# Kernel optimization log

Measured on AMD Instinct MI355X. Metric: run time of the kernel, lower is better.

The kernel has to match this reference:

```python
import jax, jax.numpy as jnp
import numpy as np

N_NODES, N_EDGES, N_GRAPHS = 50000, 800000, 512
F_IN, HID, DIM_OUT = 128, 256, 16


def setup_inputs() -> dict:
    key = jax.random.key(0)
    ks = jax.random.split(key, 16)
    glorot = lambda k, fi, fo: jax.random.normal(k, (fi, fo), jnp.float32) * jnp.sqrt(2.0 / (fi + fo))
    return {
        "x": jax.random.normal(ks[0], (N_NODES, F_IN), jnp.float32),
        "edge_index": jax.random.randint(ks[1], (2, N_EDGES), 0, N_NODES, dtype=jnp.int32),
        "batch": jnp.sort(jax.random.randint(ks[2], (N_NODES,), 0, N_GRAPHS, dtype=jnp.int32)),
        "mol_wt": jax.random.uniform(ks[3], (N_GRAPHS, 1), jnp.float32),
        "n_rings": jax.random.uniform(ks[4], (N_GRAPHS, 1), jnp.float32),
        "W1": glorot(ks[5], F_IN, HID), "b1": jnp.zeros((HID,), jnp.float32),
        "W2": glorot(ks[6], HID, HID), "b2": jnp.zeros((HID,), jnp.float32),
        "W3": glorot(ks[7], HID, HID), "b3": jnp.zeros((HID,), jnp.float32),
        "fcW1": glorot(ks[8], HID + 2, 196), "fcb1": jnp.zeros((196,), jnp.float32),
        "fcW2": glorot(ks[9], 196, DIM_OUT), "fcb2": jnp.zeros((DIM_OUT,), jnp.float32),
    }


def _gcn_conv(x, W, b, src, dst, deg_inv_sqrt, n_nodes):
    # PyG GCNConv: linear transform, then D^-1/2 (A+I) D^-1/2 aggregation, then bias
    xw = x @ W  # [N, HID]
    norm = deg_inv_sqrt[src] * deg_inv_sqrt[dst]  # [E+N]
    msg = norm[:, None] * xw[src]  # gather + scale
    out = jax.ops.segment_sum(msg, dst, num_segments=n_nodes)  # scatter-add at targets
    return out + b


def reference(x, edge_index, batch, mol_wt, n_rings,
              W1, b1, W2, b2, W3, b3, fcW1, fcb1, fcW2, fcb2):
    n_nodes = x.shape[0]
    self_loop = jnp.arange(n_nodes, dtype=edge_index.dtype)
    src = jnp.concatenate([edge_index[0], self_loop])
    dst = jnp.concatenate([edge_index[1], self_loop])
    deg = jax.ops.segment_sum(jnp.ones_like(dst, dtype=x.dtype), dst, num_segments=n_nodes)
    deg_inv_sqrt = jnp.where(deg > 0, jax.lax.rsqrt(deg), 0.0)

    h = jax.nn.relu(_gcn_conv(x, W1, b1, src, dst, deg_inv_sqrt, n_nodes))
    h = jax.nn.relu(_gcn_conv(h, W2, b2, src, dst, deg_inv_sqrt, n_nodes))
    h = jax.nn.relu(_gcn_conv(h, W3, b3, src, dst, deg_inv_sqrt, n_nodes))

    n_graphs = mol_wt.shape[0]
    sums = jax.ops.segment_sum(h, batch, num_segments=n_graphs)
    counts = jax.ops.segment_sum(jnp.ones((n_nodes,), h.dtype), batch, num_segments=n_graphs)
    hg = sums / jnp.maximum(counts, 1.0)[:, None]  # global mean pool

    hg = jnp.concatenate([hg, mol_wt, n_rings], axis=1)  # [G, 258]
    hg = jax.nn.relu(hg @ fcW1 + fcb1)
    return hg @ fcW2 + fcb2
```

## Files before the change

### kernel.cpp

```cpp
#include <hip/hip_runtime.h>

#define NN 50000
#define NE 800000
#define NG 512
#define FIN 128
#define HID 256
#define NBUK 196

typedef short short8 __attribute__((ext_vector_type(8)));
typedef float f32x4 __attribute__((ext_vector_type(4)));

static inline int cdiv(int a, int b) { return (a + b - 1) / b; }

static __device__ inline unsigned short f2bf(float f) {
    unsigned int u = __float_as_uint(f);
    unsigned int r = (u + 0x7FFF + ((u >> 16) & 1)) >> 16;
    return (unsigned short)r;
}
static __device__ inline float bf2f(unsigned short h) {
    return __uint_as_float(((unsigned int)h) << 16);
}
static __device__ inline float bflo(unsigned int p) { return __uint_as_float(p << 16); }
static __device__ inline float bfhi(unsigned int p) { return __uint_as_float(p & 0xFFFF0000u); }

typedef __attribute__((address_space(1))) unsigned int gu32;
typedef __attribute__((address_space(3))) unsigned int lu32;
static __device__ __forceinline__ void gload16(const unsigned short* g, unsigned short* l) {
    __builtin_amdgcn_global_load_lds((const gu32*)(const void*)g, (lu32*)(void*)l, 16, 0, 0);
}


__global__ __launch_bounds__(256) void hist_bucket_kernel(const int* __restrict__ dst,
                                                          int* __restrict__ gbuk) {
    __shared__ int lh[NBUK];
    int tid = threadIdx.x;
    for (int j = tid; j < NBUK; j += 256) lh[j] = 0;
    __syncthreads();
    int base = blockIdx.x * 2048;
    #pragma unroll
    for (int k = 0; k < 8; ++k) {
        int i = base + k * 256 + tid;
        if (i < NE) atomicAdd(&lh[dst[i] >> 8], 1);
    }
    __syncthreads();
    for (int j = tid; j < NBUK; j += 256) if (lh[j]) atomicAdd(&gbuk[j], lh[j]);
}

__global__ void goff_kernel(const int* __restrict__ batch, int* __restrict__ goff) {
    int i = blockIdx.x * 256 + threadIdx.x;
    if (i >= NN) return;
    int b = batch[i];
    int pb = (i == 0) ? -1 : batch[i - 1];
    for (int g = pb + 1; g <= b; ++g) goff[g] = i;
    if (i == NN - 1) for (int g = b + 1; g <= NG; ++g) goff[g] = NN;
}

__global__ void buk_scan_kernel(const int* __restrict__ gbuk, int* __restrict__ bukoff,
                                int* __restrict__ bukcur) {
    __shared__ int ws[4];
    int tid = threadIdx.x, lane = tid & 63, wid = tid >> 6;
    int v = (tid < NBUK) ? gbuk[tid] : 0;
    int incl = v;
    #pragma unroll
    for (int off = 1; off < 64; off <<= 1) {
        int u = __shfl_up(incl, off, 64);
        if (lane >= off) incl += u;
    }
    if (lane == 63) ws[wid] = incl;
    __syncthreads();
    int woff = 0;
    for (int w = 0; w < wid; ++w) woff += ws[w];
    int ex = woff + incl - v;
    if (tid < NBUK) { bukoff[tid] = ex; bukcur[tid] = ex; }
    if (tid == NBUK - 1) bukoff[NBUK] = ex + v;
}

__global__ __launch_bounds__(256) void scatter_kernel(const int* __restrict__ src,
                                                      const int* __restrict__ dst,
                                                      int* __restrict__ bukcur,
                                                      unsigned int* __restrict__ pairs) {
    __shared__ int lh[NBUK];
    __shared__ int lbase[NBUK];
    int tid = threadIdx.x;
    for (int j = tid; j < NBUK; j += 256) lh[j] = 0;
    __syncthreads();
    int base = blockIdx.x * 2048;
    int d[8], s[8];
    #pragma unroll
    for (int k = 0; k < 8; ++k) {
        int i = base + k * 256 + tid;
        if (i < NE) {
            d[k] = dst[i]; s[k] = src[i];
            atomicAdd(&lh[d[k] >> 8], 1);
        } else d[k] = -1;
    }
    __syncthreads();
    for (int j = tid; j < NBUK; j += 256) lbase[j] = lh[j] ? atomicAdd(&bukcur[j], lh[j]) : 0;
    __syncthreads();
    for (int j = tid; j < NBUK; j += 256) lh[j] = 0;
    __syncthreads();
    #pragma unroll
    for (int k = 0; k < 8; ++k) {
        if (d[k] >= 0) {
            int b = d[k] >> 8;
            int loc = atomicAdd(&lh[b], 1);
            pairs[lbase[b] + loc] = ((unsigned int)s[k] << 16) | (unsigned int)(d[k] & 255);
        }
    }
}

__global__ __launch_bounds__(256) void local_csr_kernel(const unsigned int* __restrict__ pairs,
                                                        const int* __restrict__ bukoff,
                                                        int* __restrict__ row_ptr,
                                                        int* __restrict__ col,
                                                        float* __restrict__ dis) {
    __shared__ int fcnt[256];
    __shared__ int foff[256];
    __shared__ int fws[4];
    int b = blockIdx.x, tid = threadIdx.x;
    int beg = bukoff[b], end = bukoff[b + 1];
    fcnt[tid] = 0;
    __syncthreads();
    for (int i = beg + tid; i < end; i += 256) atomicAdd(&fcnt[pairs[i] & 255], 1);
    __syncthreads();
    int lane = tid & 63, wid = tid >> 6;
    int v = fcnt[tid], incl = v;
    #pragma unroll
    for (int off = 1; off < 64; off <<= 1) {
        int u = __shfl_up(incl, off, 64);
        if (lane >= off) incl += u;
    }
    if (lane == 63) fws[wid] = incl;
    __syncthreads();
    int woff = 0;
    for (int w = 0; w < wid; ++w) woff += fws[w];
    int ex = woff + incl - v;
    foff[tid] = ex;
    int gid = b * 256 + tid;
    if (gid < NN) {
        row_ptr[gid] = beg + ex;
        dis[gid] = rsqrtf((float)v + 1.0f);
    }
    if (b == 0 && tid == 0) row_ptr[NN] = NE;
    __syncthreads();
    for (int i = beg + tid; i < end; i += 256) {
        unsigned int p = pairs[i];
        int loc = atomicAdd(&foff[p & 255], 1);
        col[beg + loc] = (int)(p >> 16);
    }
}

__global__ void cast_scale_kernel(const float* __restrict__ x, const float* __restrict__ dis,
                                  unsigned short* __restrict__ Xs, int n4) {
    int i = blockIdx.x * 256 + threadIdx.x;
    if (i < n4) {
        float dv = dis[i >> 5];
        float4 v = ((const float4*)x)[i];
        ushort4 o;
        o.x = f2bf(dv * v.x); o.y = f2bf(dv * v.y); o.z = f2bf(dv * v.z); o.w = f2bf(dv * v.w);
        ((ushort4*)Xs)[i] = o;
    }
}

__global__ void tcast_all_kernel(const float* __restrict__ W1, const float* __restrict__ W2,
                                 const float* __restrict__ W3,
                                 unsigned short* __restrict__ W1t, unsigned short* __restrict__ W2t,
                                 unsigned short* __restrict__ W3t) {
    int idx = blockIdx.x * 256 + threadIdx.x;
    if (idx < FIN * 256) {
        int n = idx / FIN, k = idx - n * FIN;
        W1t[idx] = f2bf(W1[(size_t)k * 256 + n]);
    } else if (idx < FIN * 256 + HID * 256) {
        int t = idx - FIN * 256;
        int n = t / HID, k = t - n * HID;
        W2t[t] = f2bf(W2[(size_t)k * 256 + n]);
    } else {
        int t = idx - FIN * 256 - HID * 256;
        int n = t / HID, k = t - n * HID;
        W3t[t] = f2bf(W3[(size_t)k * 256 + n]);
    }
}

template <int MODE>
__global__ __launch_bounds__(256) void gemm128_kernel(
        const unsigned short* __restrict__ A, const unsigned short* __restrict__ Bt,
        const float* __restrict__ dis, const float* __restrict__ bias,
        unsigned short* __restrict__ Cout, int M, int K) {
    __shared__ unsigned short As[128 * 32];
    __shared__ unsigned short Bs[128 * 32];
    const int tid = threadIdx.x;
    const int bm = blockIdx.x * 128, bn = blockIdx.y * 128;
    const int wave = tid >> 6, lane = tid & 63;
    const int l16 = lane & 15, quad = lane >> 4;
    const int wm = (wave & 1) * 64, wn = (wave >> 1) * 64;

    int srow0 = tid >> 2, skc = (tid & 3) * 8;
    int srow1 = (256 + tid) >> 2;
    int ar0 = bm + srow0; if (ar0 > M - 1) ar0 = M - 1;
    int ar1 = bm + srow1; if (ar1 > M - 1) ar1 = M - 1;

    f32x4 acc[4][4];
    #pragma unroll
    for (int i = 0; i < 4; ++i)
        #pragma unroll
        for (int j = 0; j < 4; ++j) acc[i][j] = (f32x4){0.f, 0.f, 0.f, 0.f};

    for (int k0 = 0; k0 < K; k0 += 32) {
        gload16(A + (size_t)ar0 * K + k0 + skc, &As[(size_t)tid * 8]);
        gload16(A + (size_t)ar1 * K + k0 + skc, &As[(size_t)(256 + tid) * 8]);
        gload16(Bt + (size_t)(bn + srow0) * K + k0 + skc, &Bs[(size_t)tid * 8]);
        gload16(Bt + (size_t)(bn + srow1) * K + k0 + skc, &Bs[(size_t)(256 + tid) * 8]);
        __syncthreads();
        short8 af[4], bf[4];
        #pragma unroll
        for (int mt = 0; mt < 4; ++mt) af[mt] = *(const short8*)&As[(wm + mt * 16 + l16) * 32 + quad * 8];
        #pragma unroll
        for (int nt = 0; nt < 4; ++nt) bf[nt] = *(const short8*)&Bs[(wn + nt * 16 + l16) * 32 + quad * 8];
        #pragma unroll
        for (int mt = 0; mt < 4; ++mt)
            #pragma unroll
            for (int nt = 0; nt < 4; ++nt)
                acc[mt][nt] = __builtin_amdgcn_mfma_f32_16x16x32_bf16(af[mt], bf[nt], acc[mt][nt], 0, 0, 0);
        __syncthreads();
    }
    float bv[4];
    #pragma unroll
    for (int nt = 0; nt < 4; ++nt) bv[nt] = bias[bn + wn + nt * 16 + l16];
    #pragma unroll
    for (int mt = 0; mt < 4; ++mt) {
        #pragma unroll
        for (int r = 0; r < 4; ++r) {
            int row = bm + wm + mt * 16 + quad * 4 + r;
            if (row < M) {
                unsigned short* crow = Cout + (size_t)row * HID + bn + wn + l16;
                if (MODE == 0) {
                    float dv = dis[row];
                    #pragma unroll
                    for (int nt = 0; nt < 4; ++nt)
                        crow[nt * 16] = f2bf(dv * fmaxf(acc[mt][nt][r] + bv[nt], 0.f));
                } else {
                    #pragma unroll
                    for (int nt = 0; nt < 4; ++nt)
                        crow[nt * 16] = f2bf(fmaxf(acc[mt][nt][r] + bv[nt], 0.f));
                }
            }
        }
    }
}

__global__ __launch_bounds__(256) void agg128_kernel(
        const unsigned short* __restrict__ Xs, const int* __restrict__ row_ptr,
        const int* __restrict__ col, const float* __restrict__ dis,
        unsigned short* __restrict__ Xa, int n) {
    int node = blockIdx.x * 4 + (threadIdx.x >> 6);
    if (node >= n) return;
    int lane = threadIdx.x & 63;
    const unsigned int* Xv = (const unsigned int*)Xs;
    unsigned int p = Xv[(size_t)node * 64 + lane];
    float ax = bflo(p), ay = bfhi(p);
    int e = row_ptr[node], end = row_ptr[node + 1];
    for (; e + 7 < end; e += 8) {
        unsigned int m[8];
        #pragma unroll
        for (int j = 0; j < 8; ++j) m[j] = Xv[(size_t)col[e + j] * 64 + lane];
        #pragma unroll
        for (int j = 0; j < 8; ++j) { ax += bflo(m[j]); ay += bfhi(m[j]); }
    }
    for (; e < end; ++e) {
        unsigned int m = Xv[(size_t)col[e] * 64 + lane];
        ax += bflo(m); ay += bfhi(m);
    }
    float dv = dis[node];
    unsigned int o = (unsigned int)f2bf(dv * ax) | ((unsigned int)f2bf(dv * ay) << 16);
    ((unsigned int*)Xa)[(size_t)node * 64 + lane] = o;
}

__global__ __launch_bounds__(256) void agg256_kernel(
        const unsigned short* __restrict__ Hs, const int* __restrict__ row_ptr,
        const int* __restrict__ col, const float* __restrict__ dis,
        unsigned short* __restrict__ G, int n) {
    int node = blockIdx.x * 4 + (threadIdx.x >> 6);
    if (node >= n) return;
    int lane = threadIdx.x & 63;
    const uint2* Hv = (const uint2*)Hs;
    uint2 p = Hv[(size_t)node * 64 + lane];
    float4 acc = make_float4(bflo(p.x), bfhi(p.x), bflo(p.y), bfhi(p.y));
    int e = row_ptr[node], end = row_ptr[node + 1];
    for (; e + 7 < end; e += 8) {
        uint2 m[8];
        #pragma unroll
        for (int j = 0; j < 8; ++j) m[j] = Hv[(size_t)col[e + j] * 64 + lane];
        #pragma unroll
        for (int j = 0; j < 8; ++j) {
            acc.x += bflo(m[j].x); acc.y += bfhi(m[j].x);
            acc.z += bflo(m[j].y); acc.w += bfhi(m[j].y);
        }
    }
    for (; e < end; ++e) {
        uint2 m = Hv[(size_t)col[e] * 64 + lane];
        acc.x += bflo(m.x); acc.y += bfhi(m.x);
        acc.z += bflo(m.y); acc.w += bfhi(m.y);
    }
    float dv = dis[node];
    ushort4 o;
    o.x = f2bf(dv * acc.x); o.y = f2bf(dv * acc.y);
    o.z = f2bf(dv * acc.z); o.w = f2bf(dv * acc.w);
    ((ushort4*)G)[(size_t)node * 64 + lane] = o;
}

__global__ __launch_bounds__(256) void pool_mlp_kernel(
        const unsigned short* __restrict__ H, const int* __restrict__ goff,
        const float* __restrict__ mol, const float* __restrict__ rings,
        const float* __restrict__ fcW1, const float* __restrict__ fcb1,
        const float* __restrict__ fcW2, const float* __restrict__ fcb2,
        float* __restrict__ out) {
    __shared__ float s_hg[258];
    __shared__ float s_t[196];
    int g = blockIdx.x, tid = threadIdx.x;
    int beg = goff[g], end = goff[g + 1];
    float acc = 0.f;
    for (int i = beg; i < end; ++i) acc += bf2f(H[(size_t)i * HID + tid]);
    s_hg[tid] = acc / fmaxf((float)(end - beg), 1.0f);
    if (tid == 0) { s_hg[256] = mol[g]; s_hg[257] = rings[g]; }
    __syncthreads();
    if (tid < 196) {
        float a = fcb1[tid];
        for (int k = 0; k < 258; ++k) a = fmaf(s_hg[k], fcW1[k * 196 + tid], a);
        s_t[tid] = fmaxf(a, 0.f);
    }
    __syncthreads();
    if (tid < 16) {
        float a = fcb2[tid];
        for (int k = 0; k < 196; ++k) a = fmaf(s_t[k], fcW2[k * 16 + tid], a);
        out[g * 16 + tid] = a;
    }
}

extern "C" void kernel_launch(void* const* d_in, const int* in_sizes, int n_in,
                              void* d_out, int out_size, void* d_ws, size_t ws_size,
                              hipStream_t stream) {
    const float* x     = (const float*)d_in[0];
    const int*   ei    = (const int*)d_in[1];
    const int*   batch = (const int*)d_in[2];
    const float* mol   = (const float*)d_in[3];
    const float* rings = (const float*)d_in[4];
    const float* W1 = (const float*)d_in[5];
    const float* b1 = (const float*)d_in[6];
    const float* W2 = (const float*)d_in[7];
    const float* b2 = (const float*)d_in[8];
    const float* W3 = (const float*)d_in[9];
    const float* b3 = (const float*)d_in[10];
    const float* fcW1 = (const float*)d_in[11];
    const float* fcb1 = (const float*)d_in[12];
    const float* fcW2 = (const float*)d_in[13];
    const float* fcb2 = (const float*)d_in[14];
    float* out = (float*)d_out;
    const int* src = ei;
    const int* dst = ei + NE;

    char* w = (char*)d_ws;
    auto alloc = [&](size_t bytes) {
        char* p = w;
        w += (bytes + 255) & ~(size_t)255;
        return p;
    };
    int*   gbuk    = (int*)alloc((size_t)NBUK * 4);
    int*   bukoff  = (int*)alloc((size_t)(NBUK + 1) * 4);
    int*   bukcur  = (int*)alloc((size_t)NBUK * 4);
    int*   row_ptr = (int*)alloc((size_t)(NN + 1) * 4);
    int*   goff    = (int*)alloc((size_t)(NG + 1) * 4);
    float* dis     = (float*)alloc((size_t)NN * 4);
    unsigned int* pairs = (unsigned int*)alloc((size_t)NE * 4);
    int*   col     = (int*)alloc((size_t)NE * 4);
    unsigned short* Xs  = (unsigned short*)alloc((size_t)NN * FIN * 2);
    unsigned short* Xa  = (unsigned short*)alloc((size_t)NN * FIN * 2);
    unsigned short* Hs  = (unsigned short*)alloc((size_t)NN * HID * 2);
    unsigned short* Ga  = (unsigned short*)alloc((size_t)NN * HID * 2);
    unsigned short* Hf  = (unsigned short*)alloc((size_t)NN * HID * 2);
    unsigned short* W1t = (unsigned short*)alloc((size_t)FIN * HID * 2);
    unsigned short* W2t = (unsigned short*)alloc((size_t)HID * HID * 2);
    unsigned short* W3t = (unsigned short*)alloc((size_t)HID * HID * 2);

    hipMemsetAsync(gbuk, 0, (size_t)NBUK * 4, stream);
    int eb = cdiv(NE, 2048);
    hist_bucket_kernel<<<eb, 256, 0, stream>>>(dst, gbuk);
    goff_kernel<<<cdiv(NN, 256), 256, 0, stream>>>(batch, goff);
    buk_scan_kernel<<<1, 256, 0, stream>>>(gbuk, bukoff, bukcur);
    scatter_kernel<<<eb, 256, 0, stream>>>(src, dst, bukcur, pairs);
    local_csr_kernel<<<NBUK, 256, 0, stream>>>(pairs, bukoff, row_ptr, col, dis);

    cast_scale_kernel<<<cdiv(NN * FIN / 4, 256), 256, 0, stream>>>(x, dis, Xs, NN * FIN / 4);
    tcast_all_kernel<<<cdiv((FIN + HID + HID) * 256, 256), 256, 0, stream>>>(W1, W2, W3, W1t, W2t, W3t);

    dim3 ggrid(cdiv(NN, 128), 2);
    int agrid = cdiv(NN, 4);
    agg128_kernel<<<agrid, 256, 0, stream>>>(Xs, row_ptr, col, dis, Xa, NN);
    gemm128_kernel<0><<<ggrid, 256, 0, stream>>>(Xa, W1t, dis, b1, Hs, NN, FIN);
    agg256_kernel<<<agrid, 256, 0, stream>>>(Hs, row_ptr, col, dis, Ga, NN);
    gemm128_kernel<0><<<ggrid, 256, 0, stream>>>(Ga, W2t, dis, b2, Hs, NN, HID);
    agg256_kernel<<<agrid, 256, 0, stream>>>(Hs, row_ptr, col, dis, Ga, NN);
    gemm128_kernel<1><<<ggrid, 256, 0, stream>>>(Ga, W3t, dis, b3, Hf, NN, HID);
    pool_mlp_kernel<<<NG, 256, 0, stream>>>(Hf, goff, mol, rings, fcW1, fcb1, fcW2, fcb2, out);
}
```

Before: 406.5 us.

## Keep weight half resident in LDS with persistent GEMM blocks over row tiles

The GEMM becomes a persistent kernel with 512 blocks. Each block loads its 128-column half of the transposed weight matrix into padded shared memory once, then loops over row tiles, streaming only A through LDS. This removes the repeated global loads of B for every K-step and every tile. In exchange each block uses about 75 KB of LDS, which limits occupancy to a couple of blocks per CU. The grid-stride tile assignment may also leave some CUs with an uneven share of the work.

```diff
diff --git a/kernel.cpp b/kernel.cpp
--- a/kernel.cpp
+++ b/kernel.cpp
@@ -6,6 +6,7 @@
 #define FIN 128
 #define HID 256
 #define NBUK 196
+#define BPAD 264
 
 typedef short short8 __attribute__((ext_vector_type(8)));
 typedef float f32x4 __attribute__((ext_vector_type(4)));
@@ -182,66 +183,76 @@
 }
 
 template <int MODE>
-__global__ __launch_bounds__(256) void gemm128_kernel(
+__global__ __launch_bounds__(256) void gemm_bres_kernel(
         const unsigned short* __restrict__ A, const unsigned short* __restrict__ Bt,
         const float* __restrict__ dis, const float* __restrict__ bias,
-        unsigned short* __restrict__ Cout, int M, int K) {
+        unsigned short* __restrict__ Cout, int M, int K, int ntiles) {
+    __shared__ unsigned short Bs[128 * BPAD];
     __shared__ unsigned short As[128 * 32];
-    __shared__ unsigned short Bs[128 * 32];
     const int tid = threadIdx.x;
-    const int bm = blockIdx.x * 128, bn = blockIdx.y * 128;
     const int wave = tid >> 6, lane = tid & 63;
     const int l16 = lane & 15, quad = lane >> 4;
     const int wm = (wave & 1) * 64, wn = (wave >> 1) * 64;
 
-    int srow0 = tid >> 2, skc = (tid & 3) * 8;
-    int srow1 = (256 + tid) >> 2;
-    int ar0 = bm + srow0; if (ar0 > M - 1) ar0 = M - 1;
-    int ar1 = bm + srow1; if (ar1 > M - 1) ar1 = M - 1;
-
-    f32x4 acc[4][4];
-    #pragma unroll
-    for (int i = 0; i < 4; ++i)
-        #pragma unroll
-        for (int j = 0; j < 4; ++j) acc[i][j] = (f32x4){0.f, 0.f, 0.f, 0.f};
-
-    for (int k0 = 0; k0 < K; k0 += 32) {
-        gload16(A + (size_t)ar0 * K + k0 + skc, &As[(size_t)tid * 8]);
-        gload16(A + (size_t)ar1 * K + k0 + skc, &As[(size_t)(256 + tid) * 8]);
-        gload16(Bt + (size_t)(bn + srow0) * K + k0 + skc, &Bs[(size_t)tid * 8]);
-        gload16(Bt + (size_t)(bn + srow1) * K + k0 + skc, &Bs[(size_t)(256 + tid) * 8]);
-        __syncthreads();
-        short8 af[4], bf[4];
-        #pragma unroll
-        for (int mt = 0; mt < 4; ++mt) af[mt] = *(const short8*)&As[(wm + mt * 16 + l16) * 32 + quad * 8];
-        #pragma unroll
-        for (int nt = 0; nt < 4; ++nt) bf[nt] = *(const short8*)&Bs[(wn + nt * 16 + l16) * 32 + quad * 8];
-        #pragma unroll
-        for (int mt = 0; mt < 4; ++mt)
+    const int nhalf = blockIdx.x & 1;
+    const int bn = nhalf * 128;
+
+    const int kc = K >> 3;
+    for (int c = tid; c < 128 * kc; c += 256) {
+        int n = c / kc, k8 = (c - n * kc) * 8;
+        *(uint4*)&Bs[n * BPAD + k8] = *(const uint4*)(Bt + (size_t)(bn + n) * K + k8);
+    }
+    float bv[4];
+    #pragma unroll
+    for (int nt = 0; nt < 4; ++nt) bv[nt] = bias[bn + wn + nt * 16 + l16];
+
+    const int srow0 = tid >> 2, skc = (tid & 3) * 8;
+    const int srow1 = (256 + tid) >> 2;
+
+    for (int t = blockIdx.x; t < ntiles; t += gridDim.x) {
+        const int bm = (t >> 1) * 128;
+        int ar0 = bm + srow0; if (ar0 > M - 1) ar0 = M - 1;
+        int ar1 = bm + srow1; if (ar1 > M - 1) ar1 = M - 1;
+
+        f32x4 acc[4][4];
+        #pragma unroll
+        for (int i = 0; i < 4; ++i)
             #pragma unroll
-            for (int nt = 0; nt < 4; ++nt)
-                acc[mt][nt] = __builtin_amdgcn_mfma_f32_16x16x32_bf16(af[mt], bf[nt], acc[mt][nt], 0, 0, 0);
-        __syncthreads();
-    }
-    float bv[4];
-    #pragma unroll
-    for (int nt = 0; nt < 4; ++nt) bv[nt] = bias[bn + wn + nt * 16 + l16];
-    #pragma unroll
-    for (int mt = 0; mt < 4; ++mt) {
-        #pragma unroll
-        for (int r = 0; r < 4; ++r) {
-            int row = bm + wm + mt * 16 + quad * 4 + r;
-            if (row < M) {
-                unsigned short* crow = Cout + (size_t)row * HID + bn + wn + l16;
-                if (MODE == 0) {
-                    float dv = dis[row];
-                    #pragma unroll
-                    for (int nt = 0; nt < 4; ++nt)
-                        crow[nt * 16] = f2bf(dv * fmaxf(acc[mt][nt][r] + bv[nt], 0.f));
-                } else {
-                    #pragma unroll
-                    for (int nt = 0; nt < 4; ++nt)
-                        crow[nt * 16] = f2bf(fmaxf(acc[mt][nt][r] + bv[nt], 0.f));
+            for (int j = 0; j < 4; ++j) acc[i][j] = (f32x4){0.f, 0.f, 0.f, 0.f};
+
+        for (int k0 = 0; k0 < K; k0 += 32) {
+            gload16(A + (size_t)ar0 * K + k0 + skc, &As[(size_t)tid * 8]);
+            gload16(A + (size_t)ar1 * K + k0 + skc, &As[(size_t)(256 + tid) * 8]);
+            __syncthreads();
+            short8 af[4], bf[4];
+            #pragma unroll
+            for (int mt = 0; mt < 4; ++mt) af[mt] = *(const short8*)&As[(wm + mt * 16 + l16) * 32 + quad * 8];
+            #pragma unroll
+            for (int nt = 0; nt < 4; ++nt) bf[nt] = *(const short8*)&Bs[(wn + nt * 16 + l16) * BPAD + k0 + quad * 8];
+            #pragma unroll
+            for (int mt = 0; mt < 4; ++mt)
+                #pragma unroll
+                for (int nt = 0; nt < 4; ++nt)
+                    acc[mt][nt] = __builtin_amdgcn_mfma_f32_16x16x32_bf16(af[mt], bf[nt], acc[mt][nt], 0, 0, 0);
+            __syncthreads();
+        }
+        #pragma unroll
+        for (int mt = 0; mt < 4; ++mt) {
+            #pragma unroll
+            for (int r = 0; r < 4; ++r) {
+                int row = bm + wm + mt * 16 + quad * 4 + r;
+                if (row < M) {
+                    unsigned short* crow = Cout + (size_t)row * HID + bn + wn + l16;
+                    if (MODE == 0) {
+                        float dv = dis[row];
+                        #pragma unroll
+                        for (int nt = 0; nt < 4; ++nt)
+                            crow[nt * 16] = f2bf(dv * fmaxf(acc[mt][nt][r] + bv[nt], 0.f));
+                    } else {
+                        #pragma unroll
+                        for (int nt = 0; nt < 4; ++nt)
+                            crow[nt * 16] = f2bf(fmaxf(acc[mt][nt][r] + bv[nt], 0.f));
+                    }
                 }
             }
         }
@@ -392,13 +403,14 @@
     cast_scale_kernel<<<cdiv(NN * FIN / 4, 256), 256, 0, stream>>>(x, dis, Xs, NN * FIN / 4);
     tcast_all_kernel<<<cdiv((FIN + HID + HID) * 256, 256), 256, 0, stream>>>(W1, W2, W3, W1t, W2t, W3t);
 
-    dim3 ggrid(cdiv(NN, 128), 2);
+    const int ntiles = cdiv(NN, 128) * 2;
+    const int ggrid = 512;
     int agrid = cdiv(NN, 4);
     agg128_kernel<<<agrid, 256, 0, stream>>>(Xs, row_ptr, col, dis, Xa, NN);
-    gemm128_kernel<0><<<ggrid, 256, 0, stream>>>(Xa, W1t, dis, b1, Hs, NN, FIN);
+    gemm_bres_kernel<0><<<ggrid, 256, 0, stream>>>(Xa, W1t, dis, b1, Hs, NN, FIN, ntiles);
     agg256_kernel<<<agrid, 256, 0, stream>>>(Hs, row_ptr, col, dis, Ga, NN);
-    gemm128_kernel<0><<<ggrid, 256, 0, stream>>>(Ga, W2t, dis, b2, Hs, NN, HID);
+    gemm_bres_kernel<0><<<ggrid, 256, 0, stream>>>(Ga, W2t, dis, b2, Hs, NN, HID, ntiles);
     agg256_kernel<<<agrid, 256, 0, stream>>>(Hs, row_ptr, col, dis, Ga, NN);
-    gemm128_kernel<1><<<ggrid, 256, 0, stream>>>(Ga, W3t, dis, b3, Hf, NN, HID);
+    gemm_bres_kernel<1><<<ggrid, 256, 0, stream>>>(Ga, W3t, dis, b3, Hf, NN, HID, ntiles);
     pool_mlp_kernel<<<NG, 256, 0, stream>>>(Hf, goff, mol, rings, fcW1, fcb1, fcW2, fcb2, out);
 }
```

Result: slower. 416.0 us (+2.4%).
